# Optimization experiments

Hardware: AMD Instinct MI355X
Metric: run time of the kernel (lower is better)

## Reference

```python
import jax, jax.numpy as jnp
import numpy as np

IN, HID, LAT, NLAYERS = 512, 256, 128, 2
B, T = 64, 512


def _init_params():
    key = jax.random.key(1)
    ks = jax.random.split(key, 24)

    def g(k, shape):
        fan_in = shape[-1]
        return (jax.random.normal(k, shape, jnp.float32) / np.sqrt(fan_in)).astype(jnp.float32)

    z = lambda n: jnp.zeros((n,), jnp.float32)
    return {
        # input projection
        'Wp': g(ks[0], (HID, IN)), 'bp': z(HID),
        # GRU layer 0 (input = hidden+latent = 384)
        'Wih0': g(ks[1], (3 * HID, HID + LAT)), 'Whh0': g(ks[2], (3 * HID, HID)),
        'bih0': z(3 * HID), 'bhh0': z(3 * HID),
        # GRU layer 1 (input = hidden)
        'Wih1': g(ks[3], (3 * HID, HID)), 'Whh1': g(ks[4], (3 * HID, HID)),
        'bih1': z(3 * HID), 'bhh1': z(3 * HID),
        # prior net
        'Wpr1': g(ks[5], (HID, HID)), 'bpr1': z(HID),
        'Wpr2': g(ks[6], (2 * LAT, HID)), 'bpr2': z(2 * LAT),
        # posterior net
        'Wpo1': g(ks[7], (HID, 2 * HID)), 'bpo1': z(HID),
        'Wpo2': g(ks[8], (2 * LAT, HID)), 'bpo2': z(2 * LAT),
        # decoder
        'Wd1': g(ks[9], (HID, HID + LAT)), 'bd1': z(HID),
        'Wd2': g(ks[10], (2 * IN, HID)), 'bd2': z(2 * IN),
    }


def setup_inputs() -> dict:
    key = jax.random.key(0)
    inp = {
        'x_seq': jax.random.normal(key, (B, T, IN), jnp.float32),
        'hidden': jnp.zeros((NLAYERS, B, HID), jnp.float32),
    }
    inp.update(_init_params())
    return inp


def _gelu(x):
    return jax.nn.gelu(x, approximate=False)  # torch default GELU is exact (erf)


def _gru_cell(x, h, Wih, Whh, bih, bhh):
    gi = x @ Wih.T + bih
    gh = h @ Whh.T + bhh
    ir, iz, inn = jnp.split(gi, 3, axis=-1)
    hr, hz, hn = jnp.split(gh, 3, axis=-1)
    r = jax.nn.sigmoid(ir + hr)
    zg = jax.nn.sigmoid(iz + hz)
    n = jnp.tanh(inn + r * hn)
    return (1.0 - zg) * n + zg * h


def _forward(x_seq, hidden, Wp, bp, Wih0, Whh0, bih0, bhh0, Wih1, Whh1, bih1, bhh1,
             Wpr1, bpr1, Wpr2, bpr2, Wpo1, bpo1, Wpo2, bpo2, Wd1, bd1, Wd2, bd2):
    x_proj = x_seq @ Wp.T + bp          # (B,T,HID)
    xs = jnp.swapaxes(x_proj, 0, 1)     # (T,B,HID)

    def step(h_carry, xt):
        h_prev = h_carry[-1]
        # prior p(z_t | h_{t-1})
        pp = _gelu(h_prev @ Wpr1.T + bpr1) @ Wpr2.T + bpr2
        p_mu, p_lv = jnp.split(pp, 2, axis=-1)
        # posterior q(z_t | h_{t-1}, x_t)
        qp = _gelu(jnp.concatenate([h_prev, xt], -1) @ Wpo1.T + bpo1) @ Wpo2.T + bpo2
        q_mu, q_lv = jnp.split(qp, 2, axis=-1)
        z_t = q_mu  # eval mode: use posterior mean
        # KL(q||p) diagonal Gaussians
        kl = 0.5 * (p_lv - q_lv + (jnp.exp(q_lv) + (q_mu - p_mu) ** 2) / jnp.exp(p_lv) - 1.0)
        kl = kl.sum(-1).mean()
        # 2-layer GRU single step
        gin = jnp.concatenate([xt, z_t], -1)
        h0 = _gru_cell(gin, h_carry[0], Wih0, Whh0, bih0, bhh0)
        h1 = _gru_cell(h0, h_carry[1], Wih1, Whh1, bih1, bhh1)
        h_new = jnp.stack([h0, h1], 0)
        # decode
        op = _gelu(jnp.concatenate([h1, z_t], -1) @ Wd1.T + bd1) @ Wd2.T + bd2
        o_mu, o_lv = jnp.split(op, 2, axis=-1)
        return h_new, (o_mu, o_lv, kl)

    hidden_f, (mus, lvs, kls) = jax.lax.scan(step, hidden, xs)
    pred_mu = jnp.swapaxes(mus, 0, 1)   # (B,T,IN)
    pred_lv = jnp.swapaxes(lvs, 0, 1)
    return pred_mu, pred_lv, kls.mean(), hidden_f


def reference(x_seq, hidden, Wp, bp, Wih0, Whh0, bih0, bhh0, Wih1, Whh1, bih1, bhh1,
              Wpr1, bpr1, Wpr2, bpr2, Wpo1, bpo1, Wpo2, bpo2, Wd1, bd1, Wd2, bd2):
    return _forward(x_seq, hidden, Wp, bp, Wih0, Whh0, bih0, bhh0, Wih1, Whh1, bih1, bhh1,
                    Wpr1, bpr1, Wpr2, bpr2, Wpo1, bpo1, Wpo2, bpo2, Wd1, bd1, Wd2, bd2)
```

## Files before the change

kernel.cpp:

```cpp
#include <hip/hip_runtime.h>
#include <math.h>

#define T_STEPS 512
#define NB      64
#define HID     256
#define IN_DIM  512
#define NWG     16

typedef __attribute__((ext_vector_type(8))) short bh8;
typedef __attribute__((ext_vector_type(4))) float f32x4;
typedef __attribute__((ext_vector_type(4))) unsigned u32x4;

#define SWZ(row, k, Kw) ((row)*(Kw) + ((k) ^ (((row)&7)*8)))

__device__ __forceinline__ float bf2f(unsigned short u) {
  union { unsigned u; float f; } v; v.u = ((unsigned)u) << 16; return v.f;
}
__device__ __forceinline__ unsigned short f2bf(float f) {
  union { float f; unsigned u; } v; v.f = f;
  unsigned r = v.u + 0x7FFFu + ((v.u >> 16) & 1u);
  return (unsigned short)(r >> 16);
}
__device__ __forceinline__ float geluf(float x) {
  return 0.5f * x * (1.f + erff(x * 0.70710678118654752f));
}
__device__ __forceinline__ float sigmf_(float x) { return 1.f / (1.f + __expf(-x)); }

__device__ __forceinline__ f32x4 mfma16(bh8 a, bh8 b, f32x4 c) {
  return __builtin_amdgcn_mfma_f32_16x16x32_bf16(a, b, c, 0, 0, 0);
}

__device__ __forceinline__ u32x4 ldt4(const unsigned* p) {
  u32x4 r;
  asm volatile("global_load_dwordx4 %0, %1, off sc0 sc1" : "=v"(r) : "v"(p));
  return r;
}
__device__ __forceinline__ void stt(unsigned* p, unsigned w) {
  asm volatile("global_store_dword %0, %1, off sc0 sc1" :: "v"(p), "v"(w) : "memory");
}

__device__ __forceinline__ void poll_unpack(const unsigned* bp, unsigned tag, bh8* out) {
  u32x4 w[16];
  for (;;) {
    #pragma unroll
    for (int j = 0; j < 8; ++j) {
      w[2*j]   = ldt4(bp + j*32);
      w[2*j+1] = ldt4(bp + j*32 + 4);
    }
    asm volatile("s_waitcnt vmcnt(0)" ::: "memory");
    unsigned acc = 0;
    #pragma unroll
    for (int i = 0; i < 16; ++i) {
      acc |= (w[i][0] ^ tag); acc |= (w[i][1] ^ tag);
      acc |= (w[i][2] ^ tag); acc |= (w[i][3] ^ tag);
    }
    if (__all((acc & 0xFFFFu) == 0u)) break;
  }
  __builtin_amdgcn_sched_barrier(0);
  #pragma unroll
  for (int j = 0; j < 8; ++j) {
    union { unsigned u[4]; bh8 v; } c;
    c.u[0] = (w[2*j][0]   >> 16) | (w[2*j][1]   & 0xFFFF0000u);
    c.u[1] = (w[2*j][2]   >> 16) | (w[2*j][3]   & 0xFFFF0000u);
    c.u[2] = (w[2*j+1][0] >> 16) | (w[2*j+1][1] & 0xFFFF0000u);
    c.u[3] = (w[2*j+1][2] >> 16) | (w[2*j+1][3] & 0xFFFF0000u);
    out[j] = c.v;
  }
}

struct PrepArgs {
  const float *hidden;
  const float *Wp, *Wpo1, *Whh0, *Whh1, *Wih1, *Wih0, *Wpo2, *Wpr1, *Wpr2, *Wd1, *Wd2;
  unsigned short *Wp_b, *Wpo1cat, *Whh0_b, *Whh1_b, *Wih1_b, *WBcat, *Wpo2_b, *Wpr1_b, *Wpr2_b, *Wd1cat, *Wd2_b;
  unsigned *H1t, *h0bt, *QPt;
};

__global__ void prep1(PrepArgs a) {
  const int task = blockIdx.y;
  const int stride = gridDim.x * blockDim.x;
  const int i0 = blockIdx.x * blockDim.x + threadIdx.x;
  switch (task) {
    case 0:  for (int i=i0;i<131072;i+=stride) a.Wp_b[i]   = f2bf(a.Wp[i]);   break;
    case 1:  for (int i=i0;i<131072;i+=stride) a.Wpo1cat[i]= f2bf(a.Wpo1[i]); break;
    case 2:  for (int i=i0;i<196608;i+=stride) a.Whh0_b[i] = f2bf(a.Whh0[i]); break;
    case 3:  for (int i=i0;i<196608;i+=stride) a.Whh1_b[i] = f2bf(a.Whh1[i]); break;
    case 4:  for (int i=i0;i<196608;i+=stride) a.Wih1_b[i] = f2bf(a.Wih1[i]); break;
    case 5:  for (int i=i0;i<196608;i+=stride) { int c=i>>8, k=i&255;
               a.WBcat[c*512+k] = f2bf(a.Wih0[c*384+k]); } break;
    case 6:  for (int i=i0;i<65536;i+=stride)  a.Wpo2_b[i] = f2bf(a.Wpo2[i]); break;
    case 7:  for (int i=i0;i<65536;i+=stride)  a.Wpr1_b[i] = f2bf(a.Wpr1[i]); break;
    case 8:  for (int i=i0;i<65536;i+=stride)  a.Wpr2_b[i] = f2bf(a.Wpr2[i]); break;
    case 9:  for (int i=i0;i<98304;i+=stride)  a.Wd1cat[i] = f2bf(a.Wd1[i]);  break;
    case 10: for (int i=i0;i<262144;i+=stride) a.Wd2_b[i]  = f2bf(a.Wd2[i]);  break;
    case 11: for (int i=i0;i<16384;i+=stride)
               a.H1t[i]  = ((unsigned)f2bf(a.hidden[16384+i])) << 16; break;
    case 12: for (int i=i0;i<16384;i+=stride)
               a.h0bt[i] = ((unsigned)f2bf(a.hidden[i])) << 16;       break;
    case 13: { u32x4 z = {0u,0u,0u,0u};
               u32x4* p = (u32x4*)a.QPt;
               for (int i=i0;i<2097152;i+=stride) p[i] = z; } break;
    case 14: { u32x4 z = {0u,0u,0u,0u};
               u32x4* p = (u32x4*)(a.H1t + 16384);
               for (int i=i0;i<2097152;i+=stride) p[i] = z; } break;
    default: break;
  }
}

__global__ void prep2(const float* __restrict__ Wih0, const float* __restrict__ Wpo2,
                      const float* __restrict__ bih0, const float* __restrict__ bpo2,
                      unsigned short* __restrict__ WBcat, float* __restrict__ bk0) {
  const int c = blockIdx.x;
  const int k = threadIdx.x;
  const float* wrow = Wih0 + c*384 + 256;
  float acc = 0.f;
  for (int j = 0; j < 128; ++j) acc += wrow[j] * Wpo2[j*256 + k];
  WBcat[c*512 + 256 + k] = f2bf(acc);
  if (k == 0) {
    float b = bih0[c];
    for (int j = 0; j < 128; ++j) b += wrow[j] * bpo2[j];
    bk0[c] = b;
  }
}

template<int FMT>
__device__ __forceinline__ void ldA(const void* A, int lda, int row, int k,
                                    unsigned short* tmp) {
  if constexpr (FMT == 1) {
    const float* p = (const float*)A + (size_t)row*lda + k;
    #pragma unroll
    for (int j = 0; j < 8; ++j) tmp[j] = f2bf(p[j]);
  } else if constexpr (FMT == 2) {
    const unsigned* p = (const unsigned*)A + (size_t)row*lda + k;
    u32x4 a0 = *(const u32x4*)p;
    u32x4 a1 = *(const u32x4*)(p + 4);
    unsigned* t32 = (unsigned*)tmp;
    t32[0] = (a0[0] >> 16) | (a0[1] & 0xFFFF0000u);
    t32[1] = (a0[2] >> 16) | (a0[3] & 0xFFFF0000u);
    t32[2] = (a1[0] >> 16) | (a1[1] & 0xFFFF0000u);
    t32[3] = (a1[2] >> 16) | (a1[3] & 0xFFFF0000u);
  } else {
    *(bh8*)tmp = *(const bh8*)((const unsigned short*)A + (size_t)row*lda + k);
  }
}

template<int EPI, int A1T, int A2T>
__global__ __launch_bounds__(256, 2) void gemm_k(
    const void* __restrict__ A1_, int lda1, int K1,
    const void* __restrict__ A2_, int lda2, int K2,
    const unsigned short* __restrict__ W, const float* __restrict__ bias,
    void* __restrict__ out_, int M, int N)
{
  __shared__ unsigned short sA[64*64];
  __shared__ unsigned short sW[64*64];
  const int m0 = blockIdx.x * 64, n0 = blockIdx.y * 64;
  const int tid = threadIdx.x, lane = tid & 63, wave = tid >> 6;
  const int Ktot = K1 + K2;
  f32x4 zero = {0.f,0.f,0.f,0.f};
  f32x4 acc[4] = {zero, zero, zero, zero};

  for (int kc = 0; kc < Ktot; kc += 64) {
    __syncthreads();
    #pragma unroll
    for (int i = 0; i < 2; ++i) {
      int cidx = tid*2 + i;
      int r = cidx >> 3, ko = (cidx & 7) * 8;
      int kg = kc + ko;
      alignas(16) unsigned short tmp[8];
      if (kg < K1) ldA<A1T>(A1_, lda1, m0 + r, kg, tmp);
      else         ldA<A2T>(A2_, lda2, m0 + r, kg - K1, tmp);
      *(bh8*)&sA[SWZ(r, ko, 64)] = *(bh8*)tmp;
    }
    #pragma unroll
    for (int i = 0; i < 2; ++i) {
      int cidx = tid*2 + i;
      int r = cidx >> 3, ko = (cidx & 7) * 8;
      const unsigned short* p = W + (size_t)(n0 + r)*Ktot + kc + ko;
      *(bh8*)&sW[SWZ(r, ko, 64)] = *(const bh8*)p;
    }
    __syncthreads();
    #pragma unroll
    for (int ks = 0; ks < 2; ++ks) {
      int k0 = ks*32 + ((lane >> 4) << 3);
      int ar = 16*wave + (lane & 15);
      bh8 a = *(const bh8*)&sA[SWZ(ar, k0, 64)];
      #pragma unroll
      for (int nt = 0; nt < 4; ++nt) {
        int wr = nt*16 + (lane & 15);
        bh8 b = *(const bh8*)&sW[SWZ(wr, k0, 64)];
        acc[nt] = mfma16(a, b, acc[nt]);
      }
    }
  }
  #pragma unroll
  for (int nt = 0; nt < 4; ++nt) {
    int col = n0 + nt*16 + (lane & 15);
    float bv = bias[col];
    #pragma unroll
    for (int r = 0; r < 4; ++r) {
      int row = m0 + 16*wave + ((lane >> 4) << 2) + r;
      float v = acc[nt][r] + bv;
      if constexpr (EPI == 0) {
        ((float*)out_)[(size_t)row*N + col] = v;
      } else if constexpr (EPI == 1) {
        ((unsigned short*)out_)[(size_t)row*N + col] = f2bf(v);
      } else if constexpr (EPI == 2) {
        int b = row >> 9, t = row & 511;
        ((unsigned short*)out_)[((size_t)t*64 + b)*N + col] = f2bf(v);
      } else if constexpr (EPI == 3) {
        ((unsigned short*)out_)[(size_t)row*N + col] = f2bf(geluf(v));
      } else {
        int t = row >> 6, b = row & 63;
        float* o = (float*)out_;
        if (col < 512) o[(size_t)b*262144 + (size_t)t*512 + col] = v;
        else o[16777216 + (size_t)b*262144 + (size_t)t*512 + (col - 512)] = v;
      }
    }
  }
}

#define SEQ_LDS_BYTES ((16*512 + 48*256 + 48*256 + 48*512 + 48*256) * 2)

__global__ __launch_bounds__(256, 1) void seq_kernel(
    const unsigned short* __restrict__ gWQ,
    const unsigned short* __restrict__ gWH0,
    const unsigned short* __restrict__ gWH1,
    const unsigned short* __restrict__ gWB,
    const unsigned short* __restrict__ gWI1,
    const float* __restrict__ bpo1, const float* __restrict__ bhh0,
    const float* __restrict__ bhh1, const float* __restrict__ bih1,
    const float* __restrict__ bk0,
    const float* __restrict__ hidden0,
    const unsigned short* __restrict__ Xp,
    unsigned* __restrict__ QPt,
    unsigned* __restrict__ H1t,
    unsigned* __restrict__ h0bt,
    float* __restrict__ outHid)
{
  extern __shared__ unsigned short lds[];
  unsigned short* WQ  = lds;
  unsigned short* WH0 = WQ  + 16*512;
  unsigned short* WH1 = WH0 + 48*256;
  unsigned short* WB  = WH1 + 48*256;
  unsigned short* WI1 = WB  + 48*512;
  const int g = blockIdx.x;
  const int tid = threadIdx.x;
  const int wave = tid >> 6, lane = tid & 63;

  for (int i = tid; i < 16*64; i += 256) { int p = i >> 6, ci = (i & 63) * 8;
    *(bh8*)&WQ[SWZ(p, ci, 512)] = *(const bh8*)&gWQ[(size_t)(16*g + p)*512 + ci]; }
  for (int i = tid; i < 48*32; i += 256) { int p = i >> 5, ci = (i & 31) * 8;
    int c = ((p >> 4) << 8) + 16*g + (p & 15);
    *(bh8*)&WH0[SWZ(p, ci, 256)] = *(const bh8*)&gWH0[(size_t)c*256 + ci]; }
  for (int i = tid; i < 48*32; i += 256) { int p = i >> 5, ci = (i & 31) * 8;
    int c = ((p >> 4) << 8) + 16*g + (p & 15);
    *(bh8*)&WH1[SWZ(p, ci, 256)] = *(const bh8*)&gWH1[(size_t)c*256 + ci]; }
  for (int i = tid; i < 48*64; i += 256) { int p = i >> 6, ci = (i & 63) * 8;
    int c = ((p >> 4) << 8) + 16*g + (p & 15);
    *(bh8*)&WB[SWZ(p, ci, 512)] = *(const bh8*)&gWB[(size_t)c*512 + ci]; }
  for (int i = tid; i < 48*32; i += 256) { int p = i >> 5, ci = (i & 31) * 8;
    int c = ((p >> 4) << 8) + 16*g + (p & 15);
    *(bh8*)&WI1[SWZ(p, ci, 256)] = *(const bh8*)&gWI1[(size_t)c*256 + ci]; }
  __syncthreads();

  const int col   = 16*g + (lane & 15);
  const int arow  = 16*wave + (lane & 15);
  const int crow0 = 16*wave + ((lane >> 4) << 2);
  const int koff  = ((lane >> 4) << 3);
  const float bq = bpo1[col];
  float bh0v[3], bh1v[3], bi1v[3], bk0v[3];
  #pragma unroll
  for (int e = 0; e < 3; ++e) {
    bh0v[e] = bhh0[e*256 + col]; bh1v[e] = bhh1[e*256 + col];
    bi1v[e] = bih1[e*256 + col]; bk0v[e] = bk0[e*256 + col];
  }
  float h0s[4], h1s[4];
  #pragma unroll
  for (int r = 0; r < 4; ++r) {
    h0s[r] = hidden0[(size_t)(crow0 + r)*HID + col];
    h1s[r] = hidden0[16384 + (size_t)(crow0 + r)*HID + col];
  }
  const f32x4 zero = {0.f,0.f,0.f,0.f};
  const int sliceoff = arow*HID + koff;

  f32x4 gh0a[3] = {zero, zero, zero};
  {
    bh8 h0i[8];
    poll_unpack(h0bt + sliceoff, 0u, h0i);
    #pragma unroll
    for (int ks = 0; ks < 8; ++ks) {
      int k0 = ks*32 + koff;
      #pragma unroll
      for (int e = 0; e < 3; ++e)
        gh0a[e] = mfma16(h0i[ks], *(const bh8*)&WH0[SWZ(e*16 + (lane&15), k0, 256)], gh0a[e]);
    }
  }
  bh8 xpr[8];
  #pragma unroll
  for (int j = 0; j < 8; ++j) xpr[j] = *(const bh8*)(Xp + (size_t)sliceoff + j*32);
  f32x4 aQ1p = zero;
  #pragma unroll
  for (int ks = 0; ks < 8; ++ks) {
    int k0 = ks*32 + koff;
    aQ1p = mfma16(xpr[ks], *(const bh8*)&WQ[SWZ(lane & 15, 256 + k0, 512)], aQ1p);
  }

  #pragma unroll 1
  for (int t = 0; t < T_STEPS; ++t) {
    const unsigned tagA = (unsigned)t;
    const unsigned tagN = (unsigned)(t + 1);
    const unsigned* h1slot = H1t + (size_t)t * (NB*HID);
    unsigned* qpslot = QPt + (size_t)t * (NB*HID);

    bh8 h1r[8];
    poll_unpack(h1slot + sliceoff, tagA, h1r);
    f32x4 aQ0 = zero;
    #pragma unroll
    for (int ks = 0; ks < 8; ++ks) {
      int k0 = ks*32 + koff;
      aQ0 = mfma16(h1r[ks], *(const bh8*)&WQ[SWZ(lane & 15, k0, 512)], aQ0);
    }
    #pragma unroll
    for (int r = 0; r < 4; ++r) {
      float v = geluf(aQ0[r] + aQ1p[r] + bq);
      stt(qpslot + (size_t)(crow0 + r)*HID + col,
          (((unsigned)f2bf(v)) << 16) | tagN);
    }
    f32x4 gh1a[3] = {zero, zero, zero};
    f32x4 gi[3]   = {zero, zero, zero};
    #pragma unroll
    for (int ks = 0; ks < 8; ++ks) {
      int k0 = ks*32 + koff;
      #pragma unroll
      for (int e = 0; e < 3; ++e) {
        gh1a[e] = mfma16(h1r[ks], *(const bh8*)&WH1[SWZ(e*16 + (lane&15), k0, 256)], gh1a[e]);
        gi[e]   = mfma16(xpr[ks], *(const bh8*)&WB[SWZ(e*16 + (lane&15), k0, 512)], gi[e]);
      }
    }

    bh8 qpr[8];
    poll_unpack(qpslot + sliceoff, tagN, qpr);
    #pragma unroll
    for (int ks = 0; ks < 8; ++ks) {
      int k0 = ks*32 + koff;
      #pragma unroll
      for (int e = 0; e < 3; ++e)
        gi[e] = mfma16(qpr[ks], *(const bh8*)&WB[SWZ(e*16 + (lane&15), 256 + k0, 512)], gi[e]);
    }
    #pragma unroll
    for (int r = 0; r < 4; ++r) {
      float rr = sigmf_(gi[0][r] + bk0v[0] + gh0a[0][r] + bh0v[0]);
      float zz = sigmf_(gi[1][r] + bk0v[1] + gh0a[1][r] + bh0v[1]);
      float nn = tanhf(gi[2][r] + bk0v[2] + rr*(gh0a[2][r] + bh0v[2]));
      float hn = (1.f - zz)*nn + zz*h0s[r];
      h0s[r] = hn;
      stt(h0bt + (size_t)(crow0 + r)*HID + col,
          (((unsigned)f2bf(hn)) << 16) | tagN);
    }
    if (t + 1 < T_STEPS) {
      const unsigned short* xq = Xp + (size_t)(t + 1) * (NB*HID);
      #pragma unroll
      for (int j = 0; j < 8; ++j) xpr[j] = *(const bh8*)(xq + (size_t)sliceoff + j*32);
    }

    bh8 h0n[8];
    poll_unpack(h0bt + sliceoff, tagN, h0n);
    f32x4 gi1[3] = {zero, zero, zero};
    #pragma unroll
    for (int ks = 0; ks < 8; ++ks) {
      int k0 = ks*32 + koff;
      #pragma unroll
      for (int e = 0; e < 3; ++e)
        gi1[e] = mfma16(h0n[ks], *(const bh8*)&WI1[SWZ(e*16 + (lane&15), k0, 256)], gi1[e]);
    }
    unsigned* h1next = H1t + (size_t)(t + 1) * (NB*HID);
    #pragma unroll
    for (int r = 0; r < 4; ++r) {
      float rr = sigmf_(gi1[0][r] + bi1v[0] + gh1a[0][r] + bh1v[0]);
      float zz = sigmf_(gi1[1][r] + bi1v[1] + gh1a[1][r] + bh1v[1]);
      float nn = tanhf(gi1[2][r] + bi1v[2] + rr*(gh1a[2][r] + bh1v[2]));
      float hv = (1.f - zz)*nn + zz*h1s[r];
      h1s[r] = hv;
      stt(h1next + (size_t)(crow0 + r)*HID + col,
          (((unsigned)f2bf(hv)) << 16) | tagN);
    }
    if (t + 1 < T_STEPS) {
      gh0a[0] = zero; gh0a[1] = zero; gh0a[2] = zero;
      aQ1p = zero;
      #pragma unroll
      for (int ks = 0; ks < 8; ++ks) {
        int k0 = ks*32 + koff;
        #pragma unroll
        for (int e = 0; e < 3; ++e)
          gh0a[e] = mfma16(h0n[ks], *(const bh8*)&WH0[SWZ(e*16 + (lane&15), k0, 256)], gh0a[e]);
        aQ1p = mfma16(xpr[ks], *(const bh8*)&WQ[SWZ(lane & 15, 256 + k0, 512)], aQ1p);
      }
    }
  }

  #pragma unroll
  for (int r = 0; r < 4; ++r) {
    int row = crow0 + r;
    outHid[(size_t)row*HID + col]         = h0s[r];
    outHid[16384 + (size_t)row*HID + col] = h1s[r];
  }
}

__global__ void kl1(const float* __restrict__ Q, const unsigned short* __restrict__ Ppb,
                    float* __restrict__ part) {
  const int m0 = blockIdx.x * 64;
  float s = 0.f;
  for (int i = threadIdx.x; i < 64*128; i += 256) {
    int m = m0 + (i >> 7), j = i & 127;
    float qm = Q[(size_t)m*256 + j],        ql = Q[(size_t)m*256 + 128 + j];
    float pm = bf2f(Ppb[(size_t)m*256 + j]), pl = bf2f(Ppb[(size_t)m*256 + 128 + j]);
    float d = qm - pm;
    s += 0.5f * (pl - ql + (expf(ql) + d*d) * expf(-pl) - 1.f);
  }
  for (int o = 32; o > 0; o >>= 1) s += __shfl_down(s, o);
  __shared__ float red[4];
  if ((threadIdx.x & 63) == 0) red[threadIdx.x >> 6] = s;
  __syncthreads();
  if (threadIdx.x == 0) part[blockIdx.x] = red[0] + red[1] + red[2] + red[3];
}
__global__ void kl2(const float* __restrict__ part, float* __restrict__ out) {
  float s = 0.f;
  for (int i = threadIdx.x; i < 512; i += 256) s += part[i];
  for (int o = 32; o > 0; o >>= 1) s += __shfl_down(s, o);
  __shared__ float red[4];
  if ((threadIdx.x & 63) == 0) red[threadIdx.x >> 6] = s;
  __syncthreads();
  if (threadIdx.x == 0) out[0] = (red[0] + red[1] + red[2] + red[3]) / 32768.f;
}

extern "C" void kernel_launch(void* const* d_in, const int* in_sizes, int n_in,
                              void* d_out, int out_size, void* d_ws, size_t ws_size,
                              hipStream_t stream) {
  const float* x_seq  = (const float*)d_in[0];
  const float* hidden = (const float*)d_in[1];
  const float* Wp   = (const float*)d_in[2];  const float* bp   = (const float*)d_in[3];
  const float* Wih0 = (const float*)d_in[4];  const float* Whh0 = (const float*)d_in[5];
  const float* bih0 = (const float*)d_in[6];  const float* bhh0 = (const float*)d_in[7];
  const float* Wih1 = (const float*)d_in[8];  const float* Whh1 = (const float*)d_in[9];
  const float* bih1 = (const float*)d_in[10]; const float* bhh1 = (const float*)d_in[11];
  const float* Wpr1 = (const float*)d_in[12]; const float* bpr1 = (const float*)d_in[13];
  const float* Wpr2 = (const float*)d_in[14]; const float* bpr2 = (const float*)d_in[15];
  const float* Wpo1 = (const float*)d_in[16]; const float* bpo1 = (const float*)d_in[17];
  const float* Wpo2 = (const float*)d_in[18]; const float* bpo2 = (const float*)d_in[19];
  const float* Wd1  = (const float*)d_in[20]; const float* bd1  = (const float*)d_in[21];
  const float* Wd2  = (const float*)d_in[22]; const float* bd2  = (const float*)d_in[23];

  char* ws = (char*)d_ws;
  char* Ob = (char*)d_out;
  float* O = (float*)d_out;

  unsigned short* Xp  = (unsigned short*)(Ob);
  unsigned*       QPt = (unsigned*)(Ob + (16u << 20));
  unsigned*       H1t = (unsigned*)(Ob + (48u << 20));
  float*          Q   = (float*)(Ob + (81u << 20));
  unsigned short* P1b = (unsigned short*)(Ob);
  unsigned short* Ppb = (unsigned short*)(Ob + (16u << 20));

  unsigned short* D1b     = (unsigned short*)(ws + 0);
  char* wb = ws + 16777216;
  unsigned short* Wp_b    = (unsigned short*)(wb + 0);
  unsigned short* Wpo1cat = (unsigned short*)(wb + 262144);
  unsigned short* Whh0_b  = (unsigned short*)(wb + 524288);
  unsigned short* Whh1_b  = (unsigned short*)(wb + 917504);
  unsigned short* Wih1_b  = (unsigned short*)(wb + 1310720);
  unsigned short* WBcat   = (unsigned short*)(wb + 1703936);
  unsigned short* Wpo2_b  = (unsigned short*)(wb + 2490368);
  unsigned short* Wpr1_b  = (unsigned short*)(wb + 2621440);
  unsigned short* Wpr2_b  = (unsigned short*)(wb + 2752512);
  unsigned short* Wd1cat  = (unsigned short*)(wb + 2883584);
  unsigned short* Wd2_b   = (unsigned short*)(wb + 3080192);
  float*    bk0   = (float*)(ws + 20381696);
  unsigned* h0bt  = (unsigned*)(ws + 20385792);
  float*    klpart= (float*)(ws + 20451328);

  PrepArgs pa;
  pa.hidden = hidden;
  pa.Wp = Wp; pa.Wpo1 = Wpo1; pa.Whh0 = Whh0; pa.Whh1 = Whh1; pa.Wih1 = Wih1;
  pa.Wih0 = Wih0; pa.Wpo2 = Wpo2; pa.Wpr1 = Wpr1; pa.Wpr2 = Wpr2; pa.Wd1 = Wd1; pa.Wd2 = Wd2;
  pa.Wp_b = Wp_b; pa.Wpo1cat = Wpo1cat; pa.Whh0_b = Whh0_b; pa.Whh1_b = Whh1_b;
  pa.Wih1_b = Wih1_b; pa.WBcat = WBcat; pa.Wpo2_b = Wpo2_b; pa.Wpr1_b = Wpr1_b;
  pa.Wpr2_b = Wpr2_b; pa.Wd1cat = Wd1cat; pa.Wd2_b = Wd2_b;
  pa.H1t = H1t; pa.h0bt = h0bt; pa.QPt = QPt;
  prep1<<<dim3(64, 15), 256, 0, stream>>>(pa);
  prep2<<<768, 256, 0, stream>>>(Wih0, Wpo2, bih0, bpo2, WBcat, bk0);

  gemm_k<2, 1, 0><<<dim3(512, 4), 256, 0, stream>>>(
      x_seq, 512, 512, nullptr, 0, 0, Wp_b, bp, Xp, 32768, 256);

  (void)hipFuncSetAttribute((const void*)seq_kernel,
                            hipFuncAttributeMaxDynamicSharedMemorySize, SEQ_LDS_BYTES);
  seq_kernel<<<NWG, 256, SEQ_LDS_BYTES, stream>>>(
      Wpo1cat, Whh0_b, Whh1_b, WBcat, Wih1_b,
      bpo1, bhh0, bhh1, bih1, bk0, hidden,
      Xp, QPt, H1t, h0bt, O + 33554433);

  gemm_k<0, 2, 0><<<dim3(512, 4), 256, 0, stream>>>(
      QPt, 256, 256, nullptr, 0, 0, Wpo2_b, bpo2, Q, 32768, 256);
  gemm_k<3, 2, 0><<<dim3(512, 4), 256, 0, stream>>>(
      H1t, 256, 256, nullptr, 0, 0, Wpr1_b, bpr1, P1b, 32768, 256);
  gemm_k<1, 0, 0><<<dim3(512, 4), 256, 0, stream>>>(
      P1b, 256, 256, nullptr, 0, 0, Wpr2_b, bpr2, Ppb, 32768, 256);
  kl1<<<512, 256, 0, stream>>>(Q, Ppb, klpart);
  kl2<<<1, 256, 0, stream>>>(klpart, O + 33554432);
  gemm_k<3, 2, 1><<<dim3(512, 4), 256, 0, stream>>>(
      H1t + 16384, 256, 256, Q, 256, 128, Wd1cat, bd1, D1b, 32768, 256);
  gemm_k<4, 0, 0><<<dim3(512, 16), 256, 0, stream>>>(
      D1b, 256, 256, nullptr, 0, 0, Wd2_b, bd2, (void*)O, 32768, 1024);

  (void)in_sizes; (void)n_in; (void)out_size; (void)ws_size;
}
```

Baseline: 5.921 ms.

## Store recurrent hidden/posterior buffers in column-chunked layout for coalesced exchange

Changes the layout of the per-step exchange buffers (h0, H1 history, QP history) from row-major to a 16-column-chunk layout, so each workgroup's stores of its 16-column slice are contiguous. Polling reads now stride by chunk, and the downstream GEMMs' FMT==2 loader is rewritten to index the new layout. The goal is fewer scattered cache lines per cross-workgroup store and poll in the latency-bound sequential loop. The risk is that polling reads become less contiguous and the later GEMM loads less regular.

```diff
diff --git a/kernel.cpp b/kernel.cpp
--- a/kernel.cpp
+++ b/kernel.cpp
@@ -13,6 +13,8 @@
 
 #define SWZ(row, k, Kw) ((row)*(Kw) + ((k) ^ (((row)&7)*8)))
 
+#define BADDR32(row, col) ((((col) >> 4) << 10) + ((row) << 4) + ((col) & 15))
+
 __device__ __forceinline__ float bf2f(unsigned short u) {
   union { unsigned u; float f; } v; v.u = ((unsigned)u) << 16; return v.f;
 }
@@ -39,13 +41,14 @@
   asm volatile("global_store_dword %0, %1, off sc0 sc1" :: "v"(p), "v"(w) : "memory");
 }
 
+#define CHSTRIDE 2048
 __device__ __forceinline__ void poll_unpack(const unsigned* bp, unsigned tag, bh8* out) {
   u32x4 w[16];
   for (;;) {
     #pragma unroll
     for (int j = 0; j < 8; ++j) {
-      w[2*j]   = ldt4(bp + j*32);
-      w[2*j+1] = ldt4(bp + j*32 + 4);
+      w[2*j]   = ldt4(bp + j*CHSTRIDE);
+      w[2*j+1] = ldt4(bp + j*CHSTRIDE + 4);
     }
     asm volatile("s_waitcnt vmcnt(0)" ::: "memory");
     unsigned acc = 0;
@@ -92,10 +95,10 @@
     case 8:  for (int i=i0;i<65536;i+=stride)  a.Wpr2_b[i] = f2bf(a.Wpr2[i]); break;
     case 9:  for (int i=i0;i<98304;i+=stride)  a.Wd1cat[i] = f2bf(a.Wd1[i]);  break;
     case 10: for (int i=i0;i<262144;i+=stride) a.Wd2_b[i]  = f2bf(a.Wd2[i]);  break;
-    case 11: for (int i=i0;i<16384;i+=stride)
-               a.H1t[i]  = ((unsigned)f2bf(a.hidden[16384+i])) << 16; break;
-    case 12: for (int i=i0;i<16384;i+=stride)
-               a.h0bt[i] = ((unsigned)f2bf(a.hidden[i])) << 16;       break;
+    case 11: for (int i=i0;i<16384;i+=stride) { int r=i>>8, c=i&255;
+               a.H1t[BADDR32(r,c)]  = ((unsigned)f2bf(a.hidden[16384+i])) << 16; } break;
+    case 12: for (int i=i0;i<16384;i+=stride) { int r=i>>8, c=i&255;
+               a.h0bt[BADDR32(r,c)] = ((unsigned)f2bf(a.hidden[i])) << 16; } break;
     case 13: { u32x4 z = {0u,0u,0u,0u};
                u32x4* p = (u32x4*)a.QPt;
                for (int i=i0;i<2097152;i+=stride) p[i] = z; } break;
@@ -130,7 +133,8 @@
     #pragma unroll
     for (int j = 0; j < 8; ++j) tmp[j] = f2bf(p[j]);
   } else if constexpr (FMT == 2) {
-    const unsigned* p = (const unsigned*)A + (size_t)row*lda + k;
+    const unsigned* p = (const unsigned*)A + ((size_t)(row >> 6))*16384
+        + (size_t)((k >> 4) << 10) + (size_t)((row & 63) << 4) + (k & 15);
     u32x4 a0 = *(const u32x4*)p;
     u32x4 a1 = *(const u32x4*)(p + 4);
     unsigned* t32 = (unsigned*)tmp;
@@ -266,6 +270,7 @@
   const int arow  = 16*wave + (lane & 15);
   const int crow0 = 16*wave + ((lane >> 4) << 2);
   const int koff  = ((lane >> 4) << 3);
+  const int l15   = lane & 15;
   const float bq = bpo1[col];
   float bh0v[3], bh1v[3], bi1v[3], bk0v[3];
   #pragma unroll
@@ -280,28 +285,29 @@
     h1s[r] = hidden0[16384 + (size_t)(crow0 + r)*HID + col];
   }
   const f32x4 zero = {0.f,0.f,0.f,0.f};
-  const int sliceoff = arow*HID + koff;
+  const int cslice = (((koff >> 4) & 1) << 10) + (arow << 4) + (koff & 8);
+  const int pst = (g << 10) + l15;
 
   f32x4 gh0a[3] = {zero, zero, zero};
   {
     bh8 h0i[8];
-    poll_unpack(h0bt + sliceoff, 0u, h0i);
+    poll_unpack(h0bt + cslice, 0u, h0i);
     #pragma unroll
     for (int ks = 0; ks < 8; ++ks) {
       int k0 = ks*32 + koff;
       #pragma unroll
       for (int e = 0; e < 3; ++e)
-        gh0a[e] = mfma16(h0i[ks], *(const bh8*)&WH0[SWZ(e*16 + (lane&15), k0, 256)], gh0a[e]);
+        gh0a[e] = mfma16(h0i[ks], *(const bh8*)&WH0[SWZ(e*16 + l15, k0, 256)], gh0a[e]);
     }
   }
   bh8 xpr[8];
   #pragma unroll
-  for (int j = 0; j < 8; ++j) xpr[j] = *(const bh8*)(Xp + (size_t)sliceoff + j*32);
+  for (int j = 0; j < 8; ++j) xpr[j] = *(const bh8*)(Xp + (size_t)arow*HID + j*32 + koff);
   f32x4 aQ1p = zero;
   #pragma unroll
   for (int ks = 0; ks < 8; ++ks) {
     int k0 = ks*32 + koff;
-    aQ1p = mfma16(xpr[ks], *(const bh8*)&WQ[SWZ(lane & 15, 256 + k0, 512)], aQ1p);
+    aQ1p = mfma16(xpr[ks], *(const bh8*)&WQ[SWZ(l15, 256 + k0, 512)], aQ1p);
   }
 
   #pragma unroll 1
@@ -312,18 +318,17 @@
     unsigned* qpslot = QPt + (size_t)t * (NB*HID);
 
     bh8 h1r[8];
-    poll_unpack(h1slot + sliceoff, tagA, h1r);
+    poll_unpack(h1slot + cslice, tagA, h1r);
     f32x4 aQ0 = zero;
     #pragma unroll
     for (int ks = 0; ks < 8; ++ks) {
       int k0 = ks*32 + koff;
-      aQ0 = mfma16(h1r[ks], *(const bh8*)&WQ[SWZ(lane & 15, k0, 512)], aQ0);
+      aQ0 = mfma16(h1r[ks], *(const bh8*)&WQ[SWZ(l15, k0, 512)], aQ0);
     }
     #pragma unroll
     for (int r = 0; r < 4; ++r) {
       float v = geluf(aQ0[r] + aQ1p[r] + bq);
-      stt(qpslot + (size_t)(crow0 + r)*HID + col,
-          (((unsigned)f2bf(v)) << 16) | tagN);
+      stt(qpslot + pst + ((crow0 + r) << 4), (((unsigned)f2bf(v)) << 16) | tagN);
     }
     f32x4 gh1a[3] = {zero, zero, zero};
     f32x4 gi[3]   = {zero, zero, zero};
@@ -332,19 +337,19 @@
       int k0 = ks*32 + koff;
       #pragma unroll
       for (int e = 0; e < 3; ++e) {
-        gh1a[e] = mfma16(h1r[ks], *(const bh8*)&WH1[SWZ(e*16 + (lane&15), k0, 256)], gh1a[e]);
-        gi[e]   = mfma16(xpr[ks], *(const bh8*)&WB[SWZ(e*16 + (lane&15), k0, 512)], gi[e]);
+        gh1a[e] = mfma16(h1r[ks], *(const bh8*)&WH1[SWZ(e*16 + l15, k0, 256)], gh1a[e]);
+        gi[e]   = mfma16(xpr[ks], *(const bh8*)&WB[SWZ(e*16 + l15, k0, 512)], gi[e]);
       }
     }
 
     bh8 qpr[8];
-    poll_unpack(qpslot + sliceoff, tagN, qpr);
+    poll_unpack(qpslot + cslice, tagN, qpr);
     #pragma unroll
     for (int ks = 0; ks < 8; ++ks) {
       int k0 = ks*32 + koff;
       #pragma unroll
       for (int e = 0; e < 3; ++e)
-        gi[e] = mfma16(qpr[ks], *(const bh8*)&WB[SWZ(e*16 + (lane&15), 256 + k0, 512)], gi[e]);
+        gi[e] = mfma16(qpr[ks], *(const bh8*)&WB[SWZ(e*16 + l15, 256 + k0, 512)], gi[e]);
     }
     #pragma unroll
     for (int r = 0; r < 4; ++r) {
@@ -353,24 +358,23 @@
       float nn = tanhf(gi[2][r] + bk0v[2] + rr*(gh0a[2][r] + bh0v[2]));
       float hn = (1.f - zz)*nn + zz*h0s[r];
       h0s[r] = hn;
-      stt(h0bt + (size_t)(crow0 + r)*HID + col,
-          (((unsigned)f2bf(hn)) << 16) | tagN);
+      stt(h0bt + pst + ((crow0 + r) << 4), (((unsigned)f2bf(hn)) << 16) | tagN);
     }
     if (t + 1 < T_STEPS) {
       const unsigned short* xq = Xp + (size_t)(t + 1) * (NB*HID);
       #pragma unroll
-      for (int j = 0; j < 8; ++j) xpr[j] = *(const bh8*)(xq + (size_t)sliceoff + j*32);
+      for (int j = 0; j < 8; ++j) xpr[j] = *(const bh8*)(xq + (size_t)arow*HID + j*32 + koff);
     }
 
     bh8 h0n[8];
-    poll_unpack(h0bt + sliceoff, tagN, h0n);
+    poll_unpack(h0bt + cslice, tagN, h0n);
     f32x4 gi1[3] = {zero, zero, zero};
     #pragma unroll
     for (int ks = 0; ks < 8; ++ks) {
       int k0 = ks*32 + koff;
       #pragma unroll
       for (int e = 0; e < 3; ++e)
-        gi1[e] = mfma16(h0n[ks], *(const bh8*)&WI1[SWZ(e*16 + (lane&15), k0, 256)], gi1[e]);
+        gi1[e] = mfma16(h0n[ks], *(const bh8*)&WI1[SWZ(e*16 + l15, k0, 256)], gi1[e]);
     }
     unsigned* h1next = H1t + (size_t)(t + 1) * (NB*HID);
     #pragma unroll
@@ -380,8 +384,7 @@
       float nn = tanhf(gi1[2][r] + bi1v[2] + rr*(gh1a[2][r] + bh1v[2]));
       float hv = (1.f - zz)*nn + zz*h1s[r];
       h1s[r] = hv;
-      stt(h1next + (size_t)(crow0 + r)*HID + col,
-          (((unsigned)f2bf(hv)) << 16) | tagN);
+      stt(h1next + pst + ((crow0 + r) << 4), (((unsigned)f2bf(hv)) << 16) | tagN);
     }
     if (t + 1 < T_STEPS) {
       gh0a[0] = zero; gh0a[1] = zero; gh0a[2] = zero;
@@ -391,8 +394,8 @@
         int k0 = ks*32 + koff;
         #pragma unroll
         for (int e = 0; e < 3; ++e)
-          gh0a[e] = mfma16(h0n[ks], *(const bh8*)&WH0[SWZ(e*16 + (lane&15), k0, 256)], gh0a[e]);
-        aQ1p = mfma16(xpr[ks], *(const bh8*)&WQ[SWZ(lane & 15, 256 + k0, 512)], aQ1p);
+          gh0a[e] = mfma16(h0n[ks], *(const bh8*)&WH0[SWZ(e*16 + l15, k0, 256)], gh0a[e]);
+        aQ1p = mfma16(xpr[ks], *(const bh8*)&WQ[SWZ(l15, 256 + k0, 512)], aQ1p);
       }
     }
   }
@@ -499,15 +502,15 @@
       Xp, QPt, H1t, h0bt, O + 33554433);
 
   gemm_k<0, 2, 0><<<dim3(512, 4), 256, 0, stream>>>(
-      QPt, 256, 256, nullptr, 0, 0, Wpo2_b, bpo2, Q, 32768, 256);
+      QPt, 0, 256, nullptr, 0, 0, Wpo2_b, bpo2, Q, 32768, 256);
   gemm_k<3, 2, 0><<<dim3(512, 4), 256, 0, stream>>>(
-      H1t, 256, 256, nullptr, 0, 0, Wpr1_b, bpr1, P1b, 32768, 256);
+      H1t, 0, 256, nullptr, 0, 0, Wpr1_b, bpr1, P1b, 32768, 256);
   gemm_k<1, 0, 0><<<dim3(512, 4), 256, 0, stream>>>(
       P1b, 256, 256, nullptr, 0, 0, Wpr2_b, bpr2, Ppb, 32768, 256);
   kl1<<<512, 256, 0, stream>>>(Q, Ppb, klpart);
   kl2<<<1, 256, 0, stream>>>(klpart, O + 33554432);
   gemm_k<3, 2, 1><<<dim3(512, 4), 256, 0, stream>>>(
-      H1t + 16384, 256, 256, Q, 256, 128, Wd1cat, bd1, D1b, 32768, 256);
+      H1t + 16384, 0, 256, Q, 256, 128, Wd1cat, bd1, D1b, 32768, 256);
   gemm_k<4, 0, 0><<<dim3(512, 16), 256, 0, stream>>>(
       D1b, 256, 256, nullptr, 0, 0, Wd2_b, bd2, (void*)O, 32768, 1024);
 
```

Result: faster. 5.052 ms (-14.7%).
